# Kernel optimization log

Hardware: AMD Instinct MI355X
Metric: run time of the kernel (lower is better)

The kernel has to match this reference:

```python
import jax, jax.numpy as jnp
import numpy as np

SEQ_LEN, BZ, D_IN = 512, 64, 1024
HIDDEN, D_OUT, NUM_LANG = 256, 1024, 16


def setup_inputs() -> dict:
    key = jax.random.key(0)
    ks = jax.random.split(key, 6)
    x = jax.random.normal(ks[0], (SEQ_LEN, BZ, D_IN), dtype=jnp.float32)
    lang_ids = jax.random.randint(ks[1], (BZ,), 0, NUM_LANG, dtype=jnp.int64)
    # Per-language 2-layer MLP params, stacked over the language axis.
    # Stored as [in, out] so y = x @ W + b (same math as torch Linear's x @ W.T + b).
    s1 = 1.0 / np.sqrt(D_IN)
    s2 = 1.0 / np.sqrt(HIDDEN)
    W1 = jax.random.uniform(ks[2], (NUM_LANG, D_IN, HIDDEN), jnp.float32, -s1, s1)
    b1 = jax.random.uniform(ks[3], (NUM_LANG, HIDDEN), jnp.float32, -s1, s1)
    W2 = jax.random.uniform(ks[4], (NUM_LANG, HIDDEN, D_OUT), jnp.float32, -s2, s2)
    b2 = jax.random.uniform(ks[5], (NUM_LANG, D_OUT), jnp.float32, -s2, s2)
    return {"x": x, "lang_ids": lang_ids, "W1": W1, "b1": b1, "W2": W2, "b2": b2}


def reference(x, lang_ids, W1, b1, W2, b2):
    # Gather each batch element's expert weights, then do batched GEMMs.
    # Equivalent to the torch loop (dispatch -> per-expert MLP -> combine),
    # without redundant gather/scatter passes.
    W1g = W1[lang_ids]            # [bz, d_in, hidden]
    b1g = b1[lang_ids]            # [bz, hidden]
    W2g = W2[lang_ids]            # [bz, hidden, d_out]
    b2g = b2[lang_ids]            # [bz, d_out]
    h = jnp.einsum('sbd,bdh->sbh', x, W1g) + b1g[None, :, :]
    h = jax.nn.relu(h)
    y = jnp.einsum('sbh,bho->sbo', h, W2g) + b2g[None, :, :]
    return y
```

## Files before the change

### kernel.cpp

```cpp
#include <hip/hip_runtime.h>

#define SEQ 512
#define BZ  64
#define DIN 1024
#define HID 256
#define DOUT 1024
#define NLANG 16

typedef __attribute__((ext_vector_type(8))) __bf16 bf16x8;
typedef __attribute__((ext_vector_type(4))) float f32x4;

__device__ __forceinline__ unsigned int f2bf_pack(float lo, float hi) {
    unsigned short a = __builtin_bit_cast(unsigned short, (__bf16)lo);
    unsigned short b = __builtin_bit_cast(unsigned short, (__bf16)hi);
    return (unsigned int)a | ((unsigned int)b << 16);
}

__global__ __launch_bounds__(256)
void transpose_cvt(const float* __restrict__ src, unsigned short* __restrict__ dst,
                   int R, int C) {
    __shared__ float tile[64][65];
    const int l  = blockIdx.x;
    const int rb = blockIdx.y * 64;
    const int cb = blockIdx.z * 64;
    const float* s = src + (long)l * R * C;
    unsigned short* d = dst + (long)l * R * C;
    const int t = threadIdx.x;
#pragma unroll
    for (int j = 0; j < 4; ++j) {
        int u = t + 256 * j;
        int r = u >> 4, c4 = u & 15;
        float4 v = *(const float4*)(s + (long)(rb + r) * C + cb + c4 * 4);
        tile[r][c4 * 4 + 0] = v.x; tile[r][c4 * 4 + 1] = v.y;
        tile[r][c4 * 4 + 2] = v.z; tile[r][c4 * 4 + 3] = v.w;
    }
    __syncthreads();
#pragma unroll
    for (int j = 0; j < 4; ++j) {
        int u = t + 256 * j;
        int dr = u >> 4, dc4 = u & 15;
        uint2 o;
        o.x = f2bf_pack(tile[dc4 * 4 + 0][dr], tile[dc4 * 4 + 1][dr]);
        o.y = f2bf_pack(tile[dc4 * 4 + 2][dr], tile[dc4 * 4 + 3][dr]);
        *(uint2*)(d + (long)(cb + dr) * R + rb + dc4 * 4) = o;
    }
}

template<int KTOT, int NTOT, bool AF32, bool L1RELU>
__global__ __launch_bounds__(256)
void mlp_gemm(const void* __restrict__ Ap,
              const unsigned short* __restrict__ Wt,
              const float* __restrict__ bias,
              const int* __restrict__ lang,
              void* __restrict__ outp) {
    __shared__ uint4 sAq[64 * 64 * 2 / 16];
    __shared__ uint4 sWq[256 * 64 * 2 / 16];
    char* sA = (char*)sAq;
    char* sW = (char*)sWq;

    const int b    = blockIdx.x;
    const int st   = blockIdx.y;
    const int nblk = blockIdx.z;
    const int t    = threadIdx.x;
    const int lane = t & 63;
    const int w    = t >> 6;
    const int lid  = lang[b];
    const int s0   = st * 64;

    const float*          Af = (const float*)Ap;
    const unsigned short* Ah = (const unsigned short*)Ap;
    const long Abase = (long)s0 * BZ * KTOT + (long)b * KTOT;
    const unsigned short* Wbase = Wt + ((long)lid * NTOT + (long)nblk * 256) * KTOT;

    const f32x4 zero4 = {0.f, 0.f, 0.f, 0.f};
    f32x4 acc[4][4];
#pragma unroll
    for (int mi = 0; mi < 4; ++mi)
#pragma unroll
        for (int ni = 0; ni < 4; ++ni) acc[mi][ni] = zero4;

    for (int kt = 0; kt < KTOT / 64; ++kt) {
        if constexpr (AF32) {
#pragma unroll
            for (int j = 0; j < 4; ++j) {
                int u = t + 256 * j;
                int m = u >> 4, c4 = u & 15;
                const float4 v = *(const float4*)(Af + Abase + (long)m * (BZ * KTOT) + kt * 64 + c4 * 4);
                uint2 p;
                p.x = f2bf_pack(v.x, v.y);
                p.y = f2bf_pack(v.z, v.w);
                *(uint2*)(sA + (((m * 128) + c4 * 8) ^ ((m & 7) << 4))) = p;
            }
        } else {
#pragma unroll
            for (int j = 0; j < 2; ++j) {
                int u = t + 256 * j;
                int m = u >> 3, c16 = u & 7;
                const uint4 v = *(const uint4*)(Ah + Abase + (long)m * (BZ * KTOT) + kt * 64 + c16 * 8);
                *(uint4*)(sA + (((m * 128) + c16 * 16) ^ ((m & 7) << 4))) = v;
            }
        }
#pragma unroll
        for (int j = 0; j < 8; ++j) {
            int u = t + 256 * j;
            int n = u >> 3, c16 = u & 7;
            const uint4 v = *(const uint4*)(Wbase + (long)n * KTOT + kt * 64 + c16 * 8);
            *(uint4*)(sW + (((n * 128) + c16 * 16) ^ ((n & 7) << 4))) = v;
        }
        __syncthreads();

#pragma unroll
        for (int ks = 0; ks < 2; ++ks) {
            const int kb = (ks * 32 + ((lane >> 4) * 8)) * 2;
            bf16x8 av[4], bv[4];
#pragma unroll
            for (int mi = 0; mi < 4; ++mi) {
                int r = mi * 16 + (lane & 15);
                av[mi] = __builtin_bit_cast(bf16x8,
                    *(const uint4*)(sA + ((r * 128 + kb) ^ ((r & 7) << 4))));
            }
#pragma unroll
            for (int ni = 0; ni < 4; ++ni) {
                int n = w * 64 + ni * 16 + (lane & 15);
                bv[ni] = __builtin_bit_cast(bf16x8,
                    *(const uint4*)(sW + ((n * 128 + kb) ^ ((n & 7) << 4))));
            }
#pragma unroll
            for (int mi = 0; mi < 4; ++mi)
#pragma unroll
                for (int ni = 0; ni < 4; ++ni)
                    acc[mi][ni] = __builtin_amdgcn_mfma_f32_16x16x32_bf16(
                        av[mi], bv[ni], acc[mi][ni], 0, 0, 0);
        }
        __syncthreads();
    }

    float bvv[4];
#pragma unroll
    for (int ni = 0; ni < 4; ++ni)
        bvv[ni] = bias[(long)lid * NTOT + nblk * 256 + w * 64 + ni * 16 + (lane & 15)];

#pragma unroll
    for (int mi = 0; mi < 4; ++mi) {
#pragma unroll
        for (int r = 0; r < 4; ++r) {
            const int  row = mi * 16 + (lane >> 4) * 4 + r;
            const long s   = s0 + row;
#pragma unroll
            for (int ni = 0; ni < 4; ++ni) {
                const int col = nblk * 256 + w * 64 + ni * 16 + (lane & 15);
                float v = acc[mi][ni][r] + bvv[ni];
                if constexpr (L1RELU) {
                    v = v > 0.f ? v : 0.f;
                    ((unsigned short*)outp)[(s * BZ + b) * NTOT + col] =
                        __builtin_bit_cast(unsigned short, (__bf16)v);
                } else {
                    ((float*)outp)[(s * BZ + b) * NTOT + col] = v;
                }
            }
        }
    }
}

extern "C" void kernel_launch(void* const* d_in, const int* in_sizes, int n_in,
                              void* d_out, int out_size, void* d_ws, size_t ws_size,
                              hipStream_t stream) {
    const float* x    = (const float*)d_in[0];
    const int*   lang = (const int*)d_in[1];
    const float* W1   = (const float*)d_in[2];
    const float* b1   = (const float*)d_in[3];
    const float* W2   = (const float*)d_in[4];
    const float* b2   = (const float*)d_in[5];
    float* y = (float*)d_out;

    const size_t w1t_bytes = (size_t)NLANG * HID * DIN * 2;
    const size_t w2t_bytes = (size_t)NLANG * DOUT * HID * 2;
    unsigned short* W1t = (unsigned short*)d_ws;
    unsigned short* W2t = (unsigned short*)((char*)d_ws + w1t_bytes);
    unsigned short* h   = (unsigned short*)((char*)d_ws + w1t_bytes + w2t_bytes);

    transpose_cvt<<<dim3(NLANG, DIN / 64, HID / 64), 256, 0, stream>>>(W1, W1t, DIN, HID);
    transpose_cvt<<<dim3(NLANG, HID / 64, DOUT / 64), 256, 0, stream>>>(W2, W2t, HID, DOUT);

    mlp_gemm<DIN, HID, true, true>
        <<<dim3(BZ, SEQ / 64, HID / 256), 256, 0, stream>>>(x, W1t, b1, lang, h);

    mlp_gemm<HID, DOUT, false, false>
        <<<dim3(BZ, SEQ / 64, DOUT / 256), 256, 0, stream>>>(h, W2t, b2, lang, y);
}
```

Measured before the change: 112.3 us.

## Pre-tile and pre-swizzle weights and hidden activations for direct global-to-LDS loads

The weight transpose kernel now writes each 256x64 tile contiguously in the already XOR-swizzled LDS layout, and layer 1 writes h in the same tiled and swizzled form. The GEMM then fills shared memory with global_load_lds 16-byte direct copies instead of loading into registers and storing to LDS. This removes VGPR staging and address math from the load path. The trade-off is scattered 2-byte writes of h in the layer-1 epilogue, and correctness depends on the direct-to-LDS per-lane placement matching the swizzle.

```diff
diff --git a/kernel.cpp b/kernel.cpp
--- a/kernel.cpp
+++ b/kernel.cpp
@@ -16,15 +16,20 @@
     return (unsigned int)a | ((unsigned int)b << 16);
 }
 
+__device__ __forceinline__ void gload_lds16(const unsigned short* g, unsigned short* l) {
+    __builtin_amdgcn_global_load_lds(
+        (const __attribute__((address_space(1))) unsigned int*)g,
+        (__attribute__((address_space(3))) unsigned int*)l, 16, 0, 0);
+}
+
 __global__ __launch_bounds__(256)
-void transpose_cvt(const float* __restrict__ src, unsigned short* __restrict__ dst,
-                   int R, int C) {
+void transpose_cvt_tile(const float* __restrict__ src, unsigned short* __restrict__ dst,
+                        int R, int C) {
     __shared__ float tile[64][65];
     const int l  = blockIdx.x;
     const int rb = blockIdx.y * 64;
     const int cb = blockIdx.z * 64;
     const float* s = src + (long)l * R * C;
-    unsigned short* d = dst + (long)l * R * C;
     const int t = threadIdx.x;
 #pragma unroll
     for (int j = 0; j < 4; ++j) {
@@ -35,28 +40,35 @@
         tile[r][c4 * 4 + 2] = v.z; tile[r][c4 * 4 + 3] = v.w;
     }
     __syncthreads();
+    const int NBl = C >> 8, KTl = R >> 6;
+    const int nb = cb >> 8, kt = rb >> 6;
+    unsigned short* dt = dst + (((long)l * NBl + nb) * KTl + kt) * 16384;
 #pragma unroll
     for (int j = 0; j < 4; ++j) {
         int u = t + 256 * j;
         int dr = u >> 4, dc4 = u & 15;
+        int n_t  = (cb & 255) + dr;
+        int ch   = dc4 >> 1, half = dc4 & 1;
         uint2 o;
         o.x = f2bf_pack(tile[dc4 * 4 + 0][dr], tile[dc4 * 4 + 1][dr]);
         o.y = f2bf_pack(tile[dc4 * 4 + 2][dr], tile[dc4 * 4 + 3][dr]);
-        *(uint2*)(d + (long)(cb + dr) * R + rb + dc4 * 4) = o;
+        *(uint2*)(dt + n_t * 64 + ((ch ^ (n_t & 7)) << 3) + half * 4) = o;
     }
 }
 
 template<int KTOT, int NTOT, bool AF32, bool L1RELU>
 __global__ __launch_bounds__(256)
 void mlp_gemm(const void* __restrict__ Ap,
-              const unsigned short* __restrict__ Wt,
+              const unsigned short* __restrict__ Ws,
               const float* __restrict__ bias,
               const int* __restrict__ lang,
               void* __restrict__ outp) {
-    __shared__ uint4 sAq[64 * 64 * 2 / 16];
-    __shared__ uint4 sWq[256 * 64 * 2 / 16];
-    char* sA = (char*)sAq;
-    char* sW = (char*)sWq;
+    constexpr int KT = KTOT / 64;
+    constexpr int NB = NTOT / 256;
+    __shared__ unsigned short sA[64 * 64];
+    __shared__ unsigned short sW[256 * 64];
+    char* cA = (char*)sA;
+    char* cW = (char*)sW;
 
     const int b    = blockIdx.x;
     const int st   = blockIdx.y;
@@ -68,9 +80,10 @@
     const int s0   = st * 64;
 
     const float*          Af = (const float*)Ap;
-    const unsigned short* Ah = (const unsigned short*)Ap;
     const long Abase = (long)s0 * BZ * KTOT + (long)b * KTOT;
-    const unsigned short* Wbase = Wt + ((long)lid * NTOT + (long)nblk * 256) * KTOT;
+    const unsigned short* At0 = (const unsigned short*)Ap
+                                + ((long)b * (SEQ / 64) + st) * KT * 4096;
+    const unsigned short* Wt0 = Ws + (((long)lid * NB + nblk) * KT) * 16384;
 
     const f32x4 zero4 = {0.f, 0.f, 0.f, 0.f};
     f32x4 acc[4][4];
@@ -79,7 +92,7 @@
 #pragma unroll
         for (int ni = 0; ni < 4; ++ni) acc[mi][ni] = zero4;
 
-    for (int kt = 0; kt < KTOT / 64; ++kt) {
+    for (int kt = 0; kt < KT; ++kt) {
         if constexpr (AF32) {
 #pragma unroll
             for (int j = 0; j < 4; ++j) {
@@ -89,23 +102,23 @@
                 uint2 p;
                 p.x = f2bf_pack(v.x, v.y);
                 p.y = f2bf_pack(v.z, v.w);
-                *(uint2*)(sA + (((m * 128) + c4 * 8) ^ ((m & 7) << 4))) = p;
+                *(uint2*)(cA + (((m * 128) + c4 * 8) ^ ((m & 7) << 4))) = p;
             }
         } else {
+            const unsigned short* At = At0 + kt * 4096;
 #pragma unroll
             for (int j = 0; j < 2; ++j) {
-                int u = t + 256 * j;
-                int m = u >> 3, c16 = u & 7;
-                const uint4 v = *(const uint4*)(Ah + Abase + (long)m * (BZ * KTOT) + kt * 64 + c16 * 8);
-                *(uint4*)(sA + (((m * 128) + c16 * 16) ^ ((m & 7) << 4))) = v;
-            }
-        }
-#pragma unroll
-        for (int j = 0; j < 8; ++j) {
-            int u = t + 256 * j;
-            int n = u >> 3, c16 = u & 7;
-            const uint4 v = *(const uint4*)(Wbase + (long)n * KTOT + kt * 64 + c16 * 8);
-            *(uint4*)(sW + (((n * 128) + c16 * 16) ^ ((n & 7) << 4))) = v;
+                int seg = w * 2 + j;
+                gload_lds16(At + seg * 512 + lane * 8, sA + seg * 512);
+            }
+        }
+        {
+            const unsigned short* Wt = Wt0 + kt * 16384;
+#pragma unroll
+            for (int j = 0; j < 8; ++j) {
+                int seg = w * 8 + j;
+                gload_lds16(Wt + seg * 512 + lane * 8, sW + seg * 512);
+            }
         }
         __syncthreads();
 
@@ -117,13 +130,13 @@
             for (int mi = 0; mi < 4; ++mi) {
                 int r = mi * 16 + (lane & 15);
                 av[mi] = __builtin_bit_cast(bf16x8,
-                    *(const uint4*)(sA + ((r * 128 + kb) ^ ((r & 7) << 4))));
+                    *(const uint4*)(cA + ((r * 128 + kb) ^ ((r & 7) << 4))));
             }
 #pragma unroll
             for (int ni = 0; ni < 4; ++ni) {
                 int n = w * 64 + ni * 16 + (lane & 15);
                 bv[ni] = __builtin_bit_cast(bf16x8,
-                    *(const uint4*)(sW + ((n * 128 + kb) ^ ((n & 7) << 4))));
+                    *(const uint4*)(cW + ((n * 128 + kb) ^ ((n & 7) << 4))));
             }
 #pragma unroll
             for (int mi = 0; mi < 4; ++mi)
@@ -144,17 +157,21 @@
     for (int mi = 0; mi < 4; ++mi) {
 #pragma unroll
         for (int r = 0; r < 4; ++r) {
-            const int  row = mi * 16 + (lane >> 4) * 4 + r;
-            const long s   = s0 + row;
+            const int row = mi * 16 + (lane >> 4) * 4 + r;
 #pragma unroll
             for (int ni = 0; ni < 4; ++ni) {
                 const int col = nblk * 256 + w * 64 + ni * 16 + (lane & 15);
                 float v = acc[mi][ni][r] + bvv[ni];
                 if constexpr (L1RELU) {
                     v = v > 0.f ? v : 0.f;
-                    ((unsigned short*)outp)[(s * BZ + b) * NTOT + col] =
+                    int kt2 = col >> 6, kk = col & 63;
+                    int ch = kk >> 3, e = kk & 7;
+                    long idx = (((long)b * (SEQ / 64) + st) * (HID / 64) + kt2) * 4096
+                             + row * 64 + ((ch ^ (row & 7)) << 3) + e;
+                    ((unsigned short*)outp)[idx] =
                         __builtin_bit_cast(unsigned short, (__bf16)v);
                 } else {
+                    const long s = s0 + row;
                     ((float*)outp)[(s * BZ + b) * NTOT + col] = v;
                 }
             }
@@ -173,18 +190,18 @@
     const float* b2   = (const float*)d_in[5];
     float* y = (float*)d_out;
 
-    const size_t w1t_bytes = (size_t)NLANG * HID * DIN * 2;
-    const size_t w2t_bytes = (size_t)NLANG * DOUT * HID * 2;
-    unsigned short* W1t = (unsigned short*)d_ws;
-    unsigned short* W2t = (unsigned short*)((char*)d_ws + w1t_bytes);
-    unsigned short* h   = (unsigned short*)((char*)d_ws + w1t_bytes + w2t_bytes);
-
-    transpose_cvt<<<dim3(NLANG, DIN / 64, HID / 64), 256, 0, stream>>>(W1, W1t, DIN, HID);
-    transpose_cvt<<<dim3(NLANG, HID / 64, DOUT / 64), 256, 0, stream>>>(W2, W2t, HID, DOUT);
+    const size_t w1s_bytes = (size_t)NLANG * HID * DIN * 2;
+    const size_t w2s_bytes = (size_t)NLANG * DOUT * HID * 2;
+    unsigned short* W1s = (unsigned short*)d_ws;
+    unsigned short* W2s = (unsigned short*)((char*)d_ws + w1s_bytes);
+    unsigned short* h   = (unsigned short*)((char*)d_ws + w1s_bytes + w2s_bytes);
+
+    transpose_cvt_tile<<<dim3(NLANG, DIN / 64, HID / 64), 256, 0, stream>>>(W1, W1s, DIN, HID);
+    transpose_cvt_tile<<<dim3(NLANG, HID / 64, DOUT / 64), 256, 0, stream>>>(W2, W2s, HID, DOUT);
 
     mlp_gemm<DIN, HID, true, true>
-        <<<dim3(BZ, SEQ / 64, HID / 256), 256, 0, stream>>>(x, W1t, b1, lang, h);
+        <<<dim3(BZ, SEQ / 64, HID / 256), 256, 0, stream>>>(x, W1s, b1, lang, h);
 
     mlp_gemm<HID, DOUT, false, false>
-        <<<dim3(BZ, SEQ / 64, DOUT / 256), 256, 0, stream>>>(h, W2t, b2, lang, y);
-}
+        <<<dim3(BZ, SEQ / 64, DOUT / 256), 256, 0, stream>>>(h, W2s, b2, lang, y);
+}
```

After: 113.1 us. No clear change (+0.8%).
